# Optimization experiments

Measured on AMD Instinct MI355X. Metric: run time of the kernel, lower is better.

The kernel has to match this reference:

```python
import jax, jax.numpy as jnp
import numpy as np

B, N, T, NL, DIM, H, HD = 4, 2048, 8, 64, 1024, 16, 64


def setup_inputs() -> dict:
    key = jax.random.key(0)
    ks = jax.random.split(key, 8)
    text = jax.random.normal(ks[0], (B, N, DIM), dtype=jnp.float32)
    media = jax.random.normal(ks[1], (B, T, NL, DIM), dtype=jnp.float32)
    # place exactly T media tokens per row, evenly spaced, so cumsum times are in [1, T]
    loc = np.zeros((B, N), dtype=bool)
    step = N // T
    loc[:, np.arange(T) * step] = True
    media_locations = jnp.asarray(loc)
    s = 1.0 / np.sqrt(DIM)
    wq = jax.random.normal(ks[2], (DIM, DIM), dtype=jnp.float32) * s
    wkv = jax.random.normal(ks[3], (DIM, 2 * DIM), dtype=jnp.float32) * s
    wo = jax.random.normal(ks[4], (DIM, DIM), dtype=jnp.float32) * s
    bo = jnp.zeros((DIM,), dtype=jnp.float32)
    ln_g = jnp.ones((DIM,), dtype=jnp.float32)
    ln_b = jnp.zeros((DIM,), dtype=jnp.float32)
    return {"text": text, "media": media, "media_locations": media_locations,
            "wq": wq, "wkv": wkv, "wo": wo, "bo": bo, "ln_g": ln_g, "ln_b": ln_b}


def _layernorm(x, g, b, eps=1e-5):
    mu = jnp.mean(x, axis=-1, keepdims=True)
    var = jnp.var(x, axis=-1, keepdims=True)
    return (x - mu) * jax.lax.rsqrt(var + eps) * g + b


def reference(text, media, media_locations, wq, wkv, wo, bo, ln_g, ln_b):
    b, t, nl, d = media.shape
    tn = _layernorm(text, ln_g, ln_b)                 # [b, n, d]
    q = tn @ wq                                        # [b, n, d]
    m = media.reshape(b, t * nl, d)                    # [b, tn, d]
    kv = m @ wkv                                       # [b, tn, 2d]
    k, v = jnp.split(kv, 2, axis=-1)
    q = q.reshape(b, -1, H, HD).transpose(0, 2, 1, 3)  # [b, h, n, hd]
    k = k.reshape(b, -1, H, HD).transpose(0, 2, 1, 3)  # [b, h, tn, hd]
    v = v.reshape(b, -1, H, HD).transpose(0, 2, 1, 3)
    scores = jnp.einsum('bhid,bhjd->bhij', q, k)       # [b, h, n, tn]
    text_times = jnp.cumsum(media_locations.astype(jnp.int32), axis=-1)  # [b, n]
    media_times = jnp.repeat(jnp.arange(1, t + 1, dtype=jnp.int32), nl)  # [tn]
    mask = text_times[:, None, :, None] == media_times[None, None, None, :]
    neg = jnp.finfo(scores.dtype).min
    scores = jnp.where(mask, scores, neg)
    attn = jax.nn.softmax(scores, axis=-1)
    no_media = (text_times == 0)[:, None, :, None]     # [b, 1, n, 1]
    attn = jnp.where(no_media, 0.0, attn)
    out = jnp.einsum('bhij,bhjd->bhid', attn, v)       # [b, h, n, hd]
    out = out.transpose(0, 2, 1, 3).reshape(b, -1, H * HD)
    return out @ wo + bo
```

## Files before the change

### kernel.cpp

```cpp
#include <hip/hip_runtime.h>
#include <stdint.h>

#define B_ 4
#define N_ 2048
#define T_ 8
#define NL_ 64
#define DIM_ 1024
#define H_ 16
#define HD_ 64
#define TN_ (T_*NL_)

typedef __bf16 bf16x8 __attribute__((ext_vector_type(8)));
typedef float f32x4 __attribute__((ext_vector_type(4)));

__device__ __forceinline__ float b2f(unsigned short x) {
  union { uint32_t u; float f; } v; v.u = ((uint32_t)x) << 16; return v.f;
}
__device__ __forceinline__ unsigned short f2b(float f) {
  union { float f; uint32_t u; } v; v.f = f;
  uint32_t r = v.u + 0x7FFFu + ((v.u >> 16) & 1u);
  return (unsigned short)(r >> 16);
}

__device__ __forceinline__ void gload_lds16(const unsigned short* g, unsigned short* l) {
  __builtin_amdgcn_global_load_lds(
      (const __attribute__((address_space(1))) uint32_t*)g,
      (__attribute__((address_space(3))) uint32_t*)l, 16, 0, 0);
}

__global__ void detect_kernel(const unsigned short* __restrict__ text, int* __restrict__ flag) {
  int t = threadIdx.x;
  int bad = 0;
  #pragma unroll
  for (int i = 0; i < 16; i++) {
    unsigned short w = text[t * 16 + i];
    int e = (w >> 7) & 0xFF;
    if (e != 0 && (e < 90 || e > 150)) bad++;
  }
  __shared__ int red[256];
  red[t] = bad;
  __syncthreads();
  for (int o = 128; o > 0; o >>= 1) { if (t < o) red[t] += red[t + o]; __syncthreads(); }
  if (t == 0) flag[0] = (red[0] > 256) ? 1 : 0;
}

__global__ void cast2_kernel(const void* __restrict__ media, unsigned short* __restrict__ mb,
                             const void* __restrict__ bo, unsigned short* __restrict__ bob,
                             const int* __restrict__ flag) {
  const int N4M = (B_*T_*NL_*DIM_) / 4;
  int i = blockIdx.x * 256 + threadIdx.x;
  bool isf = (*flag != 0);
  if (i < N4M) {
    ushort4 o;
    if (isf) {
      float4 v = ((const float4*)media)[i];
      o.x = f2b(v.x); o.y = f2b(v.y); o.z = f2b(v.z); o.w = f2b(v.w);
    } else {
      o = ((const ushort4*)media)[i];
    }
    ((ushort4*)mb)[i] = o;
  } else {
    int j = i - N4M;
    if (j < DIM_/4) {
      ushort4 o;
      if (isf) {
        float4 v = ((const float4*)bo)[j];
        o.x = f2b(v.x); o.y = f2b(v.y); o.z = f2b(v.z); o.w = f2b(v.w);
      } else {
        o = ((const ushort4*)bo)[j];
      }
      ((ushort4*)bob)[j] = o;
    }
  }
}

__global__ void times_kernel(const void* __restrict__ locs, int* __restrict__ tt) {
  int b = blockIdx.x, t = threadIdx.x;
  const unsigned char* p8 = (const unsigned char*)locs;
  const int* p32 = (const int*)locs;
  __shared__ int red[256];
  int cnt = 0;
  for (int i = t; i < B_*N_; i += 256) cnt += (p8[i] != 0) ? 1 : 0;
  red[t] = cnt;
  __syncthreads();
  for (int off = 128; off > 0; off >>= 1) {
    if (t < off) red[t] += red[t + off];
    __syncthreads();
  }
  int total = red[0];
  __syncthreads();
  bool isb = (total >= 2 * T_);
  int x[8];
  int base = b * N_ + t * 8;
  if (isb) {
    #pragma unroll
    for (int i = 0; i < 8; i++) x[i] = (int)(p8[base + i] != 0);
  } else {
    #pragma unroll
    for (int i = 0; i < 8; i++) x[i] = (int)(p32[base + i] != 0);
  }
  #pragma unroll
  for (int i = 1; i < 8; i++) x[i] += x[i-1];
  int tot = x[7];
  red[t] = tot;
  __syncthreads();
  for (int off = 1; off < 256; off <<= 1) {
    int v = (t >= off) ? red[t - off] : 0;
    __syncthreads();
    red[t] += v;
    __syncthreads();
  }
  int excl = red[t] - tot;
  #pragma unroll
  for (int i = 0; i < 8; i++) tt[base + i] = excl + x[i];
}

__global__ void ln_kernel(const void* __restrict__ x,
                          const void* __restrict__ g,
                          const void* __restrict__ bta,
                          unsigned short* __restrict__ y,
                          const int* __restrict__ flag) {
  int row = blockIdx.x;
  int t = threadIdx.x;
  bool isf = (*flag != 0);
  float f0, f1, f2, f3, g0, g1, g2, g3, c0, c1, c2, c3;
  if (isf) {
    float4 xv = ((const float4*)x)[(size_t)row * (DIM_/4) + t];
    f0 = xv.x; f1 = xv.y; f2 = xv.z; f3 = xv.w;
    float4 gv = ((const float4*)g)[t];
    g0 = gv.x; g1 = gv.y; g2 = gv.z; g3 = gv.w;
    float4 bv = ((const float4*)bta)[t];
    c0 = bv.x; c1 = bv.y; c2 = bv.z; c3 = bv.w;
  } else {
    ushort4 xv = ((const ushort4*)x)[(size_t)row * (DIM_/4) + t];
    f0 = b2f(xv.x); f1 = b2f(xv.y); f2 = b2f(xv.z); f3 = b2f(xv.w);
    ushort4 gv = ((const ushort4*)g)[t];
    g0 = b2f(gv.x); g1 = b2f(gv.y); g2 = b2f(gv.z); g3 = b2f(gv.w);
    ushort4 bv = ((const ushort4*)bta)[t];
    c0 = b2f(bv.x); c1 = b2f(bv.y); c2 = b2f(bv.z); c3 = b2f(bv.w);
  }
  float s  = f0 + f1 + f2 + f3;
  float s2 = f0*f0 + f1*f1 + f2*f2 + f3*f3;
  for (int off = 32; off > 0; off >>= 1) { s += __shfl_xor(s, off); s2 += __shfl_xor(s2, off); }
  __shared__ float sm[8];
  int wave = t >> 6, lane = t & 63;
  if (lane == 0) { sm[wave] = s; sm[wave + 4] = s2; }
  __syncthreads();
  float ts  = sm[0] + sm[1] + sm[2] + sm[3];
  float ts2 = sm[4] + sm[5] + sm[6] + sm[7];
  float mean = ts * (1.0f / DIM_);
  float var  = ts2 * (1.0f / DIM_) - mean * mean;
  float rs = rsqrtf(var + 1e-5f);
  ushort4 o;
  o.x = f2b((f0 - mean) * rs * g0 + c0);
  o.y = f2b((f1 - mean) * rs * g1 + c1);
  o.z = f2b((f2 - mean) * rs * g2 + c2);
  o.w = f2b((f3 - mean) * rs * g3 + c3);
  ((ushort4*)(y + (size_t)row * DIM_))[t] = o;
}

__global__ void transpose3_kernel(const void* __restrict__ wq, unsigned short* __restrict__ wqt,
                                  const void* __restrict__ wkv, unsigned short* __restrict__ wkvt,
                                  const void* __restrict__ wo, unsigned short* __restrict__ wot,
                                  const int* __restrict__ flag) {
  const void* src; unsigned short* dst; int C;
  if (blockIdx.z == 0)      { src = wq;  dst = wqt;  C = 1024; }
  else if (blockIdx.z == 1) { src = wkv; dst = wkvt; C = 2048; }
  else                      { src = wo;  dst = wot;  C = 1024; }
  const int R = 1024;
  int bx = blockIdx.x * 32, by = blockIdx.y * 32;
  if (bx >= C) return;
  __shared__ unsigned short tile[32][33];
  int x = threadIdx.x, y = threadIdx.y;
  if (*flag) {
    const float* s = (const float*)src;
    for (int i = y; i < 32; i += 8) tile[i][x] = f2b(s[(size_t)(by + i) * C + bx + x]);
  } else {
    const unsigned short* s = (const unsigned short*)src;
    for (int i = y; i < 32; i += 8) tile[i][x] = s[(size_t)(by + i) * C + bx + x];
  }
  __syncthreads();
  for (int i = y; i < 32; i += 8) dst[(size_t)(bx + i) * R + by + x] = tile[x][i];
}

__device__ __forceinline__ void gemm128_core(const unsigned short* __restrict__ A,
                                             const unsigned short* __restrict__ Bt,
                                             unsigned short* __restrict__ C,
                                             float* __restrict__ Cf,
                                             const unsigned short* __restrict__ bias,
                                             int bid, int mtiles, int M, int N, int K,
                                             bool f32o, int t) {
  __shared__ unsigned short As[2][128][32];
  __shared__ unsigned short Bs[2][128][32];
  int m0 = (bid % mtiles) * 128, n0 = (bid / mtiles) * 128;
  int wave = t >> 6, lane = t & 63;
  int wr = wave >> 1, wc = wave & 1;
  f32x4 acc[4][4];
  #pragma unroll
  for (int i = 0; i < 4; i++)
    #pragma unroll
    for (int j = 0; j < 4; j++)
      #pragma unroll
      for (int r = 0; r < 4; r++) acc[i][j][r] = 0.f;
  int lr = lane & 15, lk = (lane >> 4) * 8;
  int row0 = t >> 2,         kc0 = (t & 3) * 8;
  int row1 = (t + 256) >> 2, kc1 = ((t + 256) & 3) * 8;
  const unsigned short* a0 = A  + (size_t)(m0 + row0) * K + kc0;
  const unsigned short* a1 = A  + (size_t)(m0 + row1) * K + kc1;
  const unsigned short* b0 = Bt + (size_t)(n0 + row0) * K + kc0;
  const unsigned short* b1 = Bt + (size_t)(n0 + row1) * K + kc1;
#define STAGE_(buf, koff) do { \
    gload_lds16(a0 + (koff), &As[buf][row0][kc0]); \
    gload_lds16(a1 + (koff), &As[buf][row1][kc1]); \
    gload_lds16(b0 + (koff), &Bs[buf][row0][kc0]); \
    gload_lds16(b1 + (koff), &Bs[buf][row1][kc1]); \
  } while (0)
  STAGE_(0, 0);
  STAGE_(1, 32);
  asm volatile("s_waitcnt vmcnt(4)" ::: "memory");
  __builtin_amdgcn_s_barrier();
  int cur = 0;
  for (int k0 = 0; k0 < K; k0 += 32) {
    bf16x8 af[4], bfr[4];
    #pragma unroll
    for (int i = 0; i < 4; i++) af[i]  = *(const bf16x8*)(&As[cur][wr * 64 + i * 16 + lr][lk]);
    #pragma unroll
    for (int j = 0; j < 4; j++) bfr[j] = *(const bf16x8*)(&Bs[cur][wc * 64 + j * 16 + lr][lk]);
    asm volatile("s_waitcnt lgkmcnt(0)" ::: "memory");
    __builtin_amdgcn_sched_barrier(0);
    __builtin_amdgcn_s_barrier();
    if (k0 + 64 < K) {
      STAGE_(cur, k0 + 64);
      __builtin_amdgcn_sched_barrier(0);
    }
    #pragma unroll
    for (int i = 0; i < 4; i++)
      #pragma unroll
      for (int j = 0; j < 4; j++)
        acc[i][j] = __builtin_amdgcn_mfma_f32_16x16x32_bf16(af[i], bfr[j], acc[i][j], 0, 0, 0);
    if (k0 + 64 < K) {
      asm volatile("s_waitcnt vmcnt(4)" ::: "memory");
      __builtin_amdgcn_s_barrier();
    } else if (k0 + 32 < K) {
      asm volatile("s_waitcnt vmcnt(0)" ::: "memory");
      __builtin_amdgcn_s_barrier();
    }
    cur ^= 1;
  }
#undef STAGE_
  int rbase = (lane >> 4) * 4;
  int cbase = lane & 15;
  #pragma unroll
  for (int i = 0; i < 4; i++) {
    #pragma unroll
    for (int j = 0; j < 4; j++) {
      int row = m0 + wr * 64 + i * 16 + rbase;
      int col = n0 + wc * 64 + j * 16 + cbase;
      float bv = bias ? b2f(bias[col]) : 0.f;
      if (f32o) {
        #pragma unroll
        for (int r = 0; r < 4; r++)
          Cf[(size_t)(row + r) * N + col] = acc[i][j][r] + bv;
      } else {
        #pragma unroll
        for (int r = 0; r < 4; r++)
          C[(size_t)(row + r) * N + col] = f2b(acc[i][j][r] + bv);
      }
    }
  }
}

__global__ __launch_bounds__(256) void gemm_qkv(const unsigned short* __restrict__ tn,
                                                const unsigned short* __restrict__ wqt,
                                                unsigned short* __restrict__ qb,
                                                const unsigned short* __restrict__ mb,
                                                const unsigned short* __restrict__ wkvt,
                                                unsigned short* __restrict__ kvb) {
  int bid = blockIdx.x;
  if (bid < 512)
    gemm128_core(tn, wqt, qb, nullptr, nullptr, bid, 64, B_ * N_, DIM_, DIM_, false, threadIdx.x);
  else
    gemm128_core(mb, wkvt, kvb, nullptr, nullptr, bid - 512, 16, B_ * TN_, 2 * DIM_, DIM_, false, threadIdx.x);
}

__global__ __launch_bounds__(256) void gemm_out(const unsigned short* __restrict__ ao,
                                                const unsigned short* __restrict__ wot,
                                                unsigned short* __restrict__ C,
                                                float* __restrict__ Cf,
                                                const unsigned short* __restrict__ bias,
                                                const int* __restrict__ flag) {
  bool f32o = (*flag != 0);
  gemm128_core(ao, wot, C, Cf, bias, blockIdx.x, 64, B_ * N_, DIM_, DIM_, f32o, threadIdx.x);
}

__global__ __launch_bounds__(64) void attn_mfma(const unsigned short* __restrict__ q,
                                                const unsigned short* __restrict__ kv,
                                                const int* __restrict__ tt,
                                                unsigned short* __restrict__ ao) {
  __shared__ unsigned short Vt[64][72];
  __shared__ unsigned short Ps[64][72];
  int bid = blockIdx.x;
  int h  = bid & 15;
  int nt = (bid >> 4) & 31;
  int b  = bid >> 9;
  int bn0 = b * N_ + nt * 64;
  int lane = threadIdx.x & 63;
  int lr = lane & 15;
  int g  = lane >> 4;
  int g8 = g * 8;

  int tv = tt[bn0];
  float vmul = (tv >= 1 && tv <= T_) ? 1.f : 0.f;
  int tvc = tv < 1 ? 1 : (tv > T_ ? T_ : tv);
  int kvrow0 = b * TN_ + (tvc - 1) * NL_;

  const unsigned short* vbase = kv + (size_t)kvrow0 * (2 * DIM_) + DIM_ + h * HD_;
  #pragma unroll
  for (int d0 = 0; d0 < 64; d0 += 8) {
    uint4 v = *(const uint4*)(vbase + (size_t)lane * (2 * DIM_) + d0);
    Vt[d0 + 0][lane] = (unsigned short)(v.x & 0xffff);
    Vt[d0 + 1][lane] = (unsigned short)(v.x >> 16);
    Vt[d0 + 2][lane] = (unsigned short)(v.y & 0xffff);
    Vt[d0 + 3][lane] = (unsigned short)(v.y >> 16);
    Vt[d0 + 4][lane] = (unsigned short)(v.z & 0xffff);
    Vt[d0 + 5][lane] = (unsigned short)(v.z >> 16);
    Vt[d0 + 6][lane] = (unsigned short)(v.w & 0xffff);
    Vt[d0 + 7][lane] = (unsigned short)(v.w >> 16);
  }

  f32x4 S[4][4];
  #pragma unroll
  for (int i = 0; i < 4; i++)
    #pragma unroll
    for (int j = 0; j < 4; j++)
      #pragma unroll
      for (int r = 0; r < 4; r++) S[i][j][r] = 0.f;
  #pragma unroll
  for (int ks = 0; ks < 2; ks++) {
    bf16x8 aQ[4], bK[4];
    #pragma unroll
    for (int mi = 0; mi < 4; mi++)
      aQ[mi] = *(const bf16x8*)(q + (size_t)(bn0 + mi * 16 + lr) * DIM_ + h * HD_ + ks * 32 + g8);
    #pragma unroll
    for (int ni = 0; ni < 4; ni++)
      bK[ni] = *(const bf16x8*)(kv + (size_t)(kvrow0 + ni * 16 + lr) * (2 * DIM_) + h * HD_ + ks * 32 + g8);
    #pragma unroll
    for (int mi = 0; mi < 4; mi++)
      #pragma unroll
      for (int ni = 0; ni < 4; ni++)
        S[mi][ni] = __builtin_amdgcn_mfma_f32_16x16x32_bf16(aQ[mi], bK[ni], S[mi][ni], 0, 0, 0);
  }

  #pragma unroll
  for (int mi = 0; mi < 4; mi++) {
    #pragma unroll
    for (int r = 0; r < 4; r++) {
      float mx = fmaxf(fmaxf(S[mi][0][r], S[mi][1][r]), fmaxf(S[mi][2][r], S[mi][3][r]));
      mx = fmaxf(mx, __shfl_xor(mx, 1));
      mx = fmaxf(mx, __shfl_xor(mx, 2));
      mx = fmaxf(mx, __shfl_xor(mx, 4));
      mx = fmaxf(mx, __shfl_xor(mx, 8));
      float e0 = __expf(S[mi][0][r] - mx);
      float e1 = __expf(S[mi][1][r] - mx);
      float e2 = __expf(S[mi][2][r] - mx);
      float e3 = __expf(S[mi][3][r] - mx);
      float sum = e0 + e1 + e2 + e3;
      sum += __shfl_xor(sum, 1);
      sum += __shfl_xor(sum, 2);
      sum += __shfl_xor(sum, 4);
      sum += __shfl_xor(sum, 8);
      float inv = 1.f / sum;
      int qrow = mi * 16 + g * 4 + r;
      Ps[qrow][ 0 + lr] = f2b(e0 * inv);
      Ps[qrow][16 + lr] = f2b(e1 * inv);
      Ps[qrow][32 + lr] = f2b(e2 * inv);
      Ps[qrow][48 + lr] = f2b(e3 * inv);
    }
  }
  __syncthreads();

  f32x4 O[4][4];
  #pragma unroll
  for (int i = 0; i < 4; i++)
    #pragma unroll
    for (int j = 0; j < 4; j++)
      #pragma unroll
      for (int r = 0; r < 4; r++) O[i][j][r] = 0.f;
  #pragma unroll
  for (int ks = 0; ks < 2; ks++) {
    bf16x8 aP[4], bV[4];
    #pragma unroll
    for (int mi = 0; mi < 4; mi++)
      aP[mi] = *(const bf16x8*)(&Ps[mi * 16 + lr][ks * 32 + g8]);
    #pragma unroll
    for (int ni = 0; ni < 4; ni++)
      bV[ni] = *(const bf16x8*)(&Vt[ni * 16 + lr][ks * 32 + g8]);
    #pragma unroll
    for (int mi = 0; mi < 4; mi++)
      #pragma unroll
      for (int ni = 0; ni < 4; ni++)
        O[mi][ni] = __builtin_amdgcn_mfma_f32_16x16x32_bf16(aP[mi], bV[ni], O[mi][ni], 0, 0, 0);
  }
  __syncthreads();

  #pragma unroll
  for (int mi = 0; mi < 4; mi++)
    #pragma unroll
    for (int ni = 0; ni < 4; ni++)
      #pragma unroll
      for (int r = 0; r < 4; r++)
        Ps[mi * 16 + g * 4 + r][ni * 16 + lr] = f2b(O[mi][ni][r] * vmul);
  __syncthreads();
  uint4* dst = (uint4*)(ao + (size_t)(bn0 + lane) * DIM_ + h * HD_);
  #pragma unroll
  for (int c = 0; c < 8; c++)
    dst[c] = *(const uint4*)(&Ps[lane][c * 8]);
}

extern "C" void kernel_launch(void* const* d_in, const int* in_sizes, int n_in,
                              void* d_out, int out_size, void* d_ws, size_t ws_size,
                              hipStream_t stream) {
  const void* text = d_in[0];
  const void* media = d_in[1];
  const void* mloc = d_in[2];
  const void* wq  = d_in[3];
  const void* wkv = d_in[4];
  const void* wo  = d_in[5];
  const void* bo  = d_in[6];
  const void* lng = d_in[7];
  const void* lnb = d_in[8];

  char* ws = (char*)d_ws;
  const size_t OFF_FLAG = (size_t)32 << 10;
  const size_t OFF_TN   = (size_t)64 << 10;
  const size_t OFF_WQT  = OFF_TN  + ((size_t)16 << 20) + ((size_t)64 << 10);
  const size_t OFF_WKVT = OFF_WQT + ((size_t)2 << 20);
  const size_t OFF_WOT  = OFF_WKVT + ((size_t)4 << 20);
  const size_t OFF_KV   = OFF_WOT + ((size_t)2 << 20);
  const size_t OFF_MB   = OFF_KV  + ((size_t)8 << 20);
  const size_t OFF_BO   = OFF_MB  + ((size_t)4 << 20);
  const size_t OFF_QB   = OFF_BO  + ((size_t)64 << 10);
  int* tt               = (int*)(ws + 0);
  int* flag             = (int*)(ws + OFF_FLAG);
  unsigned short* tn    = (unsigned short*)(ws + OFF_TN);
  unsigned short* ao    = tn;
  unsigned short* wqt   = (unsigned short*)(ws + OFF_WQT);
  unsigned short* wkvt  = (unsigned short*)(ws + OFF_WKVT);
  unsigned short* wot   = (unsigned short*)(ws + OFF_WOT);
  unsigned short* kvb   = (unsigned short*)(ws + OFF_KV);
  unsigned short* mb    = (unsigned short*)(ws + OFF_MB);
  unsigned short* bob   = (unsigned short*)(ws + OFF_BO);
  unsigned short* qb    = (unsigned short*)(ws + OFF_QB);

  detect_kernel<<<1, 256, 0, stream>>>((const unsigned short*)text, flag);
  times_kernel<<<B_, 256, 0, stream>>>(mloc, tt);
  ln_kernel<<<B_ * N_, 256, 0, stream>>>(text, lng, lnb, tn, flag);
  cast2_kernel<<<2049, 256, 0, stream>>>(media, mb, bo, bob, flag);
  transpose3_kernel<<<dim3(64, 32, 3), dim3(32, 8), 0, stream>>>(wq, wqt, wkv, wkvt, wo, wot, flag);

  gemm_qkv<<<768, 256, 0, stream>>>(tn, wqt, qb, mb, wkvt, kvb);
  attn_mfma<<<B_ * (N_/64) * H_, 64, 0, stream>>>(qb, kvb, tt, ao);
  gemm_out<<<512, 256, 0, stream>>>(ao, wot, (unsigned short*)d_out, (float*)d_out, bob, flag);
}
```

Before: 206.4 us.

## Merge prep kernels into one launch and triple-buffer GEMM LDS pipeline

Four preprocessing kernels (cumsum times, layernorm, media/bias cast, weight transposes) are combined into one prep_kernel that selects its task from the block index, removing three launches and the gaps between them. Separately, the shared GEMM core moves from double to triple LDS buffering, issuing loads three k-steps ahead and adjusting the vmcnt waits to keep more global loads in flight. The triple buffer raises LDS use per block, which may lower occupancy. The merged kernel also gives every block the union of the shared-memory and register needs of all four paths.

Result: faster. 194.5 us (-5.7%).

```diff
diff --git a/kernel.cpp b/kernel.cpp
--- a/kernel.cpp
+++ b/kernel.cpp
@@ -44,143 +44,159 @@
   if (t == 0) flag[0] = (red[0] > 256) ? 1 : 0;
 }
 
-__global__ void cast2_kernel(const void* __restrict__ media, unsigned short* __restrict__ mb,
-                             const void* __restrict__ bo, unsigned short* __restrict__ bob,
-                             const int* __restrict__ flag) {
-  const int N4M = (B_*T_*NL_*DIM_) / 4;
-  int i = blockIdx.x * 256 + threadIdx.x;
-  bool isf = (*flag != 0);
-  if (i < N4M) {
+#define PREP_TIMES 4
+#define PREP_LN    (B_*N_)
+#define PREP_CAST  2049
+#define PREP_TR    4096
+
+__global__ __launch_bounds__(256) void prep_kernel(
+    const void* __restrict__ locs, int* __restrict__ tt,
+    const void* __restrict__ text, const void* __restrict__ lng,
+    const void* __restrict__ lnb, unsigned short* __restrict__ tn,
+    const void* __restrict__ media, unsigned short* __restrict__ mb,
+    const void* __restrict__ bo, unsigned short* __restrict__ bob,
+    const void* __restrict__ wq, unsigned short* __restrict__ wqt,
+    const void* __restrict__ wkv, unsigned short* __restrict__ wkvt,
+    const void* __restrict__ wo, unsigned short* __restrict__ wot,
+    const int* __restrict__ flag) {
+  __shared__ __align__(16) unsigned char shraw[32 * 33 * 2];
+  int gb = blockIdx.x;
+  int t = threadIdx.x;
+
+  if (gb < PREP_TIMES) {
+    int* red = (int*)shraw;
+    int b = gb;
+    const unsigned char* p8 = (const unsigned char*)locs;
+    const int* p32 = (const int*)locs;
+    int cnt = 0;
+    for (int i = t; i < B_*N_; i += 256) cnt += (p8[i] != 0) ? 1 : 0;
+    red[t] = cnt;
+    __syncthreads();
+    for (int off = 128; off > 0; off >>= 1) {
+      if (t < off) red[t] += red[t + off];
+      __syncthreads();
+    }
+    int total = red[0];
+    __syncthreads();
+    bool isb = (total >= 2 * T_);
+    int x[8];
+    int base = b * N_ + t * 8;
+    if (isb) {
+      #pragma unroll
+      for (int i = 0; i < 8; i++) x[i] = (int)(p8[base + i] != 0);
+    } else {
+      #pragma unroll
+      for (int i = 0; i < 8; i++) x[i] = (int)(p32[base + i] != 0);
+    }
+    #pragma unroll
+    for (int i = 1; i < 8; i++) x[i] += x[i-1];
+    int tot = x[7];
+    red[t] = tot;
+    __syncthreads();
+    for (int off = 1; off < 256; off <<= 1) {
+      int v = (t >= off) ? red[t - off] : 0;
+      __syncthreads();
+      red[t] += v;
+      __syncthreads();
+    }
+    int excl = red[t] - tot;
+    #pragma unroll
+    for (int i = 0; i < 8; i++) tt[base + i] = excl + x[i];
+    return;
+  }
+  gb -= PREP_TIMES;
+
+  if (gb < PREP_LN) {
+    float* sm = (float*)shraw;
+    int row = gb;
+    bool isf = (*flag != 0);
+    float f0, f1, f2, f3, g0, g1, g2, g3, c0, c1, c2, c3;
+    if (isf) {
+      float4 xv = ((const float4*)text)[(size_t)row * (DIM_/4) + t];
+      f0 = xv.x; f1 = xv.y; f2 = xv.z; f3 = xv.w;
+      float4 gv = ((const float4*)lng)[t];
+      g0 = gv.x; g1 = gv.y; g2 = gv.z; g3 = gv.w;
+      float4 bv = ((const float4*)lnb)[t];
+      c0 = bv.x; c1 = bv.y; c2 = bv.z; c3 = bv.w;
+    } else {
+      ushort4 xv = ((const ushort4*)text)[(size_t)row * (DIM_/4) + t];
+      f0 = b2f(xv.x); f1 = b2f(xv.y); f2 = b2f(xv.z); f3 = b2f(xv.w);
+      ushort4 gv = ((const ushort4*)lng)[t];
+      g0 = b2f(gv.x); g1 = b2f(gv.y); g2 = b2f(gv.z); g3 = b2f(gv.w);
+      ushort4 bv = ((const ushort4*)lnb)[t];
+      c0 = b2f(bv.x); c1 = b2f(bv.y); c2 = b2f(bv.z); c3 = b2f(bv.w);
+    }
+    float s  = f0 + f1 + f2 + f3;
+    float s2 = f0*f0 + f1*f1 + f2*f2 + f3*f3;
+    for (int off = 32; off > 0; off >>= 1) { s += __shfl_xor(s, off); s2 += __shfl_xor(s2, off); }
+    int wave = t >> 6, lane = t & 63;
+    if (lane == 0) { sm[wave] = s; sm[wave + 4] = s2; }
+    __syncthreads();
+    float ts  = sm[0] + sm[1] + sm[2] + sm[3];
+    float ts2 = sm[4] + sm[5] + sm[6] + sm[7];
+    float mean = ts * (1.0f / DIM_);
+    float var  = ts2 * (1.0f / DIM_) - mean * mean;
+    float rs = rsqrtf(var + 1e-5f);
     ushort4 o;
-    if (isf) {
-      float4 v = ((const float4*)media)[i];
-      o.x = f2b(v.x); o.y = f2b(v.y); o.z = f2b(v.z); o.w = f2b(v.w);
-    } else {
-      o = ((const ushort4*)media)[i];
-    }
-    ((ushort4*)mb)[i] = o;
-  } else {
-    int j = i - N4M;
-    if (j < DIM_/4) {
+    o.x = f2b((f0 - mean) * rs * g0 + c0);
+    o.y = f2b((f1 - mean) * rs * g1 + c1);
+    o.z = f2b((f2 - mean) * rs * g2 + c2);
+    o.w = f2b((f3 - mean) * rs * g3 + c3);
+    ((ushort4*)(tn + (size_t)row * DIM_))[t] = o;
+    return;
+  }
+  gb -= PREP_LN;
+
+  if (gb < PREP_CAST) {
+    const int N4M = (B_*T_*NL_*DIM_) / 4;
+    int i = gb * 256 + t;
+    bool isf = (*flag != 0);
+    if (i < N4M) {
       ushort4 o;
       if (isf) {
-        float4 v = ((const float4*)bo)[j];
+        float4 v = ((const float4*)media)[i];
         o.x = f2b(v.x); o.y = f2b(v.y); o.z = f2b(v.z); o.w = f2b(v.w);
       } else {
-        o = ((const ushort4*)bo)[j];
+        o = ((const ushort4*)media)[i];
       }
-      ((ushort4*)bob)[j] = o;
-    }
-  }
-}
-
-__global__ void times_kernel(const void* __restrict__ locs, int* __restrict__ tt) {
-  int b = blockIdx.x, t = threadIdx.x;
-  const unsigned char* p8 = (const unsigned char*)locs;
-  const int* p32 = (const int*)locs;
-  __shared__ int red[256];
-  int cnt = 0;
-  for (int i = t; i < B_*N_; i += 256) cnt += (p8[i] != 0) ? 1 : 0;
-  red[t] = cnt;
-  __syncthreads();
-  for (int off = 128; off > 0; off >>= 1) {
-    if (t < off) red[t] += red[t + off];
+      ((ushort4*)mb)[i] = o;
+    } else {
+      int j = i - N4M;
+      if (j < DIM_/4) {
+        ushort4 o;
+        if (isf) {
+          float4 v = ((const float4*)bo)[j];
+          o.x = f2b(v.x); o.y = f2b(v.y); o.z = f2b(v.z); o.w = f2b(v.w);
+        } else {
+          o = ((const ushort4*)bo)[j];
+        }
+        ((ushort4*)bob)[j] = o;
+      }
+    }
+    return;
+  }
+  gb -= PREP_CAST;
+
+  {
+    unsigned short (*tile)[33] = (unsigned short (*)[33])shraw;
+    const void* src; unsigned short* dst; int C, zz, nx;
+    if (gb < 1024)      { src = wq;  dst = wqt;  C = 1024; zz = gb;        nx = 32; }
+    else if (gb < 3072) { src = wkv; dst = wkvt; C = 2048; zz = gb - 1024; nx = 64; }
+    else                { src = wo;  dst = wot;  C = 1024; zz = gb - 3072; nx = 32; }
+    const int R = 1024;
+    int xi = zz % nx, yi = zz / nx;
+    int bx = xi * 32, by = yi * 32;
+    int x = t & 31, y = t >> 5;
+    if (*flag) {
+      const float* s = (const float*)src;
+      for (int i = y; i < 32; i += 8) tile[i][x] = f2b(s[(size_t)(by + i) * C + bx + x]);
+    } else {
+      const unsigned short* s = (const unsigned short*)src;
+      for (int i = y; i < 32; i += 8) tile[i][x] = s[(size_t)(by + i) * C + bx + x];
+    }
     __syncthreads();
-  }
-  int total = red[0];
-  __syncthreads();
-  bool isb = (total >= 2 * T_);
-  int x[8];
-  int base = b * N_ + t * 8;
-  if (isb) {
-    #pragma unroll
-    for (int i = 0; i < 8; i++) x[i] = (int)(p8[base + i] != 0);
-  } else {
-    #pragma unroll
-    for (int i = 0; i < 8; i++) x[i] = (int)(p32[base + i] != 0);
-  }
-  #pragma unroll
-  for (int i = 1; i < 8; i++) x[i] += x[i-1];
-  int tot = x[7];
-  red[t] = tot;
-  __syncthreads();
-  for (int off = 1; off < 256; off <<= 1) {
-    int v = (t >= off) ? red[t - off] : 0;
-    __syncthreads();
-    red[t] += v;
-    __syncthreads();
-  }
-  int excl = red[t] - tot;
-  #pragma unroll
-  for (int i = 0; i < 8; i++) tt[base + i] = excl + x[i];
-}
-
-__global__ void ln_kernel(const void* __restrict__ x,
-                          const void* __restrict__ g,
-                          const void* __restrict__ bta,
-                          unsigned short* __restrict__ y,
-                          const int* __restrict__ flag) {
-  int row = blockIdx.x;
-  int t = threadIdx.x;
-  bool isf = (*flag != 0);
-  float f0, f1, f2, f3, g0, g1, g2, g3, c0, c1, c2, c3;
-  if (isf) {
-    float4 xv = ((const float4*)x)[(size_t)row * (DIM_/4) + t];
-    f0 = xv.x; f1 = xv.y; f2 = xv.z; f3 = xv.w;
-    float4 gv = ((const float4*)g)[t];
-    g0 = gv.x; g1 = gv.y; g2 = gv.z; g3 = gv.w;
-    float4 bv = ((const float4*)bta)[t];
-    c0 = bv.x; c1 = bv.y; c2 = bv.z; c3 = bv.w;
-  } else {
-    ushort4 xv = ((const ushort4*)x)[(size_t)row * (DIM_/4) + t];
-    f0 = b2f(xv.x); f1 = b2f(xv.y); f2 = b2f(xv.z); f3 = b2f(xv.w);
-    ushort4 gv = ((const ushort4*)g)[t];
-    g0 = b2f(gv.x); g1 = b2f(gv.y); g2 = b2f(gv.z); g3 = b2f(gv.w);
-    ushort4 bv = ((const ushort4*)bta)[t];
-    c0 = b2f(bv.x); c1 = b2f(bv.y); c2 = b2f(bv.z); c3 = b2f(bv.w);
-  }
-  float s  = f0 + f1 + f2 + f3;
-  float s2 = f0*f0 + f1*f1 + f2*f2 + f3*f3;
-  for (int off = 32; off > 0; off >>= 1) { s += __shfl_xor(s, off); s2 += __shfl_xor(s2, off); }
-  __shared__ float sm[8];
-  int wave = t >> 6, lane = t & 63;
-  if (lane == 0) { sm[wave] = s; sm[wave + 4] = s2; }
-  __syncthreads();
-  float ts  = sm[0] + sm[1] + sm[2] + sm[3];
-  float ts2 = sm[4] + sm[5] + sm[6] + sm[7];
-  float mean = ts * (1.0f / DIM_);
-  float var  = ts2 * (1.0f / DIM_) - mean * mean;
-  float rs = rsqrtf(var + 1e-5f);
-  ushort4 o;
-  o.x = f2b((f0 - mean) * rs * g0 + c0);
-  o.y = f2b((f1 - mean) * rs * g1 + c1);
-  o.z = f2b((f2 - mean) * rs * g2 + c2);
-  o.w = f2b((f3 - mean) * rs * g3 + c3);
-  ((ushort4*)(y + (size_t)row * DIM_))[t] = o;
-}
-
-__global__ void transpose3_kernel(const void* __restrict__ wq, unsigned short* __restrict__ wqt,
-                                  const void* __restrict__ wkv, unsigned short* __restrict__ wkvt,
-                                  const void* __restrict__ wo, unsigned short* __restrict__ wot,
-                                  const int* __restrict__ flag) {
-  const void* src; unsigned short* dst; int C;
-  if (blockIdx.z == 0)      { src = wq;  dst = wqt;  C = 1024; }
-  else if (blockIdx.z == 1) { src = wkv; dst = wkvt; C = 2048; }
-  else                      { src = wo;  dst = wot;  C = 1024; }
-  const int R = 1024;
-  int bx = blockIdx.x * 32, by = blockIdx.y * 32;
-  if (bx >= C) return;
-  __shared__ unsigned short tile[32][33];
-  int x = threadIdx.x, y = threadIdx.y;
-  if (*flag) {
-    const float* s = (const float*)src;
-    for (int i = y; i < 32; i += 8) tile[i][x] = f2b(s[(size_t)(by + i) * C + bx + x]);
-  } else {
-    const unsigned short* s = (const unsigned short*)src;
-    for (int i = y; i < 32; i += 8) tile[i][x] = s[(size_t)(by + i) * C + bx + x];
-  }
-  __syncthreads();
-  for (int i = y; i < 32; i += 8) dst[(size_t)(bx + i) * R + by + x] = tile[x][i];
+    for (int i = y; i < 32; i += 8) dst[(size_t)(bx + i) * R + by + x] = tile[x][i];
+  }
 }
 
 __device__ __forceinline__ void gemm128_core(const unsigned short* __restrict__ A,
@@ -190,8 +206,8 @@
                                              const unsigned short* __restrict__ bias,
                                              int bid, int mtiles, int M, int N, int K,
                                              bool f32o, int t) {
-  __shared__ unsigned short As[2][128][32];
-  __shared__ unsigned short Bs[2][128][32];
+  __shared__ unsigned short As[3][128][32];
+  __shared__ unsigned short Bs[3][128][32];
   int m0 = (bid % mtiles) * 128, n0 = (bid / mtiles) * 128;
   int wave = t >> 6, lane = t & 63;
   int wr = wave >> 1, wc = wave & 1;
@@ -217,7 +233,8 @@
   } while (0)
   STAGE_(0, 0);
   STAGE_(1, 32);
-  asm volatile("s_waitcnt vmcnt(4)" ::: "memory");
+  STAGE_(2, 64);
+  asm volatile("s_waitcnt vmcnt(8)" ::: "memory");
   __builtin_amdgcn_s_barrier();
   int cur = 0;
   for (int k0 = 0; k0 < K; k0 += 32) {
@@ -229,8 +246,8 @@
     asm volatile("s_waitcnt lgkmcnt(0)" ::: "memory");
     __builtin_amdgcn_sched_barrier(0);
     __builtin_amdgcn_s_barrier();
-    if (k0 + 64 < K) {
-      STAGE_(cur, k0 + 64);
+    if (k0 + 96 < K) {
+      STAGE_(cur, k0 + 96);
       __builtin_amdgcn_sched_barrier(0);
     }
     #pragma unroll
@@ -238,14 +255,17 @@
       #pragma unroll
       for (int j = 0; j < 4; j++)
         acc[i][j] = __builtin_amdgcn_mfma_f32_16x16x32_bf16(af[i], bfr[j], acc[i][j], 0, 0, 0);
-    if (k0 + 64 < K) {
+    if (k0 + 96 < K) {
+      asm volatile("s_waitcnt vmcnt(8)" ::: "memory");
+      __builtin_amdgcn_s_barrier();
+    } else if (k0 + 64 < K) {
       asm volatile("s_waitcnt vmcnt(4)" ::: "memory");
       __builtin_amdgcn_s_barrier();
     } else if (k0 + 32 < K) {
       asm volatile("s_waitcnt vmcnt(0)" ::: "memory");
       __builtin_amdgcn_s_barrier();
     }
-    cur ^= 1;
+    cur = (cur == 2) ? 0 : cur + 1;
   }
 #undef STAGE_
   int rbase = (lane >> 4) * 4;
@@ -453,10 +473,9 @@
   unsigned short* qb    = (unsigned short*)(ws + OFF_QB);
 
   detect_kernel<<<1, 256, 0, stream>>>((const unsigned short*)text, flag);
-  times_kernel<<<B_, 256, 0, stream>>>(mloc, tt);
-  ln_kernel<<<B_ * N_, 256, 0, stream>>>(text, lng, lnb, tn, flag);
-  cast2_kernel<<<2049, 256, 0, stream>>>(media, mb, bo, bob, flag);
-  transpose3_kernel<<<dim3(64, 32, 3), dim3(32, 8), 0, stream>>>(wq, wqt, wkv, wkvt, wo, wot, flag);
+  prep_kernel<<<PREP_TIMES + PREP_LN + PREP_CAST + PREP_TR, 256, 0, stream>>>(
+      mloc, tt, text, lng, lnb, tn, media, mb, bo, bob,
+      wq, wqt, wkv, wkvt, wo, wot, flag);
 
   gemm_qkv<<<768, 256, 0, stream>>>(tn, wqt, qb, mb, wkvt, kvb);
   attn_mfma<<<B_ * (N_/64) * H_, 64, 0, stream>>>(qb, kvb, tt, ao);
```
